# Kernel optimization log

Measured on AMD Instinct MI355X. Metric: run time of the kernel, lower is better.

## Reference

```python
import jax, jax.numpy as jnp
import numpy as np

BS, N = 8, 2000
ALPHA = 0.2  # LeakyReLU slope
NEG = -9e15


def _gat_head(x, adj, W, a):
    # x: [bs,N,Fin], W: [Fin,Fout], a: [2*Fout]
    h = x @ W                                   # [bs,N,F]
    F_ = W.shape[-1]
    # e_ij = lrelu(h_i . a[:F] + h_j . a[F:])  (decomposed form of concat+matmul)
    src = h @ a[:F_]                            # [bs,N]
    dst = h @ a[F_:]                            # [bs,N]
    e = jax.nn.leaky_relu(src[:, :, None] + dst[:, None, :], ALPHA)  # [bs,N,N]
    att = jnp.where(adj[None] > 0, e, NEG)
    att = jax.nn.softmax(att, axis=-1)
    return jax.nn.elu(att @ h)                  # [bs,N,F]


def _gat_multihead(x, adj, W, a):
    # W: [H,Fin,Fout], a: [H,2*Fout] -> concat heads on feature dim
    out = jax.vmap(_gat_head, in_axes=(None, None, 0, 0))(x, adj, W, a)  # [H,bs,N,F]
    H, bs, n, F_ = out.shape
    return jnp.moveaxis(out, 0, 2).reshape(bs, n, H * F_)


def setup_inputs() -> dict:
    key = jax.random.key(0)
    ks = jax.random.split(key, 20)
    g = 1.414

    def xavu(k, shape, gain=1.0):
        fan_in, fan_out = shape[-2], shape[-1]
        lim = gain * np.sqrt(6.0 / (fan_in + fan_out))
        return jax.random.uniform(k, shape, jnp.float32, -lim, lim)

    x = jax.random.normal(ks[0], (BS, N, 1), jnp.float32)
    adj = jax.random.randint(ks[1], (N, N), 0, 2).astype(jnp.float32)
    inp = {
        "x": x, "adj": adj,
        "W1": xavu(ks[2], (4, 1, 8), g), "a1": xavu(ks[3], (4, 16, 1), g)[..., 0],
        "W2": xavu(ks[4], (3, 32, 16), g), "a2": xavu(ks[5], (3, 32, 1), g)[..., 0],
        "pw1": xavu(ks[6], (32, 1))[:, 0], "pb1": jnp.zeros((1,), jnp.float32),
        "pw2": xavu(ks[7], (48, 1))[:, 0], "pb2": jnp.zeros((1,), jnp.float32),
        "fc1_w": xavu(ks[8], (3 * N, 600)), "fc1_b": jnp.zeros((600,), jnp.float32),
        "fc2_w": xavu(ks[9], (600, 256)), "fc2_b": jnp.zeros((256,), jnp.float32),
        "fc3_w": xavu(ks[10], (256, 64)), "fc3_b": jnp.zeros((64,), jnp.float32),
        "fc4_w": xavu(ks[11], (64, 32)), "fc4_b": jnp.zeros((32,), jnp.float32),
        "fc5_w": xavu(ks[12], (32, 2)), "fc5_b": jnp.zeros((2,), jnp.float32),
    }
    return inp


def reference(x, adj, W1, a1, W2, a2, pw1, pb1, pw2, pb2,
              fc1_w, fc1_b, fc2_w, fc2_b, fc3_w, fc3_b, fc4_w, fc4_b, fc5_w, fc5_b):
    # dropout layers are identity in eval mode
    x0 = jnp.mean(x, axis=-1)                       # [bs,N]
    h = _gat_multihead(x, adj, W1, a1)              # [bs,N,32]
    x1 = h @ pw1 + pb1                              # [bs,N]
    h = _gat_multihead(h, adj, W2, a2)              # [bs,N,48]
    x2 = h @ pw2 + pb2                              # [bs,N]
    z = jnp.concatenate([x0, x1, x2], axis=1)       # [bs,3N]
    z = jax.nn.elu(z @ fc1_w + fc1_b)
    z = jax.nn.elu(z @ fc2_w + fc2_b)
    z1 = jax.nn.elu(z @ fc3_w + fc3_b)              # output [bs,64]
    z = jax.nn.elu(z1 @ fc4_w + fc4_b)
    gat_out = z @ fc5_w + fc5_b                     # [bs,2]
    return (z1, gat_out)
```

## Files before the change

### kernel.cpp

```cpp
#include <hip/hip_runtime.h>
#include <hip/hip_bf16.h>
#include <cmath>

#define N_NODES 2000
#define BS 8

typedef __attribute__((ext_vector_type(8))) short short8v;
typedef __attribute__((ext_vector_type(4))) float float4v;

__device__ __forceinline__ float elu_f(float v) { return v > 0.f ? v : expm1f(v); }

__device__ __forceinline__ unsigned short f32_bf16u(float f) {
    __hip_bfloat16 h = __float2bfloat16(f);
    unsigned short u;
    __builtin_memcpy(&u, &h, 2);
    return u;
}
__device__ __forceinline__ short f32_bf16(float f) { return (short)f32_bf16u(f); }

__device__ __forceinline__ float sel_mask(float w, unsigned long long m) {
    float r;
    asm("v_cndmask_b32 %0, 0, %1, %2" : "=v"(r) : "v"(w), "s"(m));
    return r;
}

__global__ __launch_bounds__(256) void pack_kernel(
    const float* __restrict__ adj,
    unsigned long long* __restrict__ maskT, unsigned* __restrict__ maskT32,
    short* __restrict__ hT) {
    int bx = blockIdx.x;
    int tid = threadIdx.x;
    if (bx < N_NODES) {
        int row = bx;
        int lane = tid & 63, wv = tid >> 6;
        for (int wq = wv; wq < 32; wq += 4) {
            int j = wq * 64 + lane;
            bool on = (j < N_NODES) && (adj[(size_t)row * N_NODES + j] > 0.f);
            unsigned long long bal = __ballot(on);
            if (lane == 0) {
                maskT[(size_t)wq * 2048 + row] = bal;
                maskT32[(size_t)(2 * wq) * 2048 + row] = (unsigned)bal;
                maskT32[(size_t)(2 * wq + 1) * 2048 + row] = (unsigned)(bal >> 32);
            }
        }
        return;
    }
    for (int i = tid; i < 24 * 16 * 48; i += 256) {
        int bh = i / 768, rem = i % 768, f = rem / 48, n = N_NODES + rem % 48;
        hT[((size_t)bh * 16 + f) * 2048 + n] = 0;
    }
}

__global__ __launch_bounds__(256) void att1_kernel(
    const unsigned long long* __restrict__ maskT,
    const float* __restrict__ x,
    const float* __restrict__ W1, const float* __restrict__ a1,
    float* __restrict__ o1) {
    __shared__ unsigned sPQ[2][2048];
    __shared__ float sX[2048];
    __shared__ float2 redmm[256];
    int tid = threadIdx.x;
    int by = blockIdx.y, b = blockIdx.z;

    float mn = 1e30f, mx = -1e30f;
    for (int n = tid; n < 2048; n += 256) {
        float xv = (n < N_NODES) ? x[(size_t)b * N_NODES + n] : 0.f;
        sX[n] = xv;
        if (n < N_NODES) { mn = fminf(mn, xv); mx = fmaxf(mx, xv); }
    }
    redmm[tid] = make_float2(mn, mx);
    __syncthreads();
    for (int s = 128; s > 0; s >>= 1) {
        if (tid < s) {
            redmm[tid].x = fminf(redmm[tid].x, redmm[tid + s].x);
            redmm[tid].y = fmaxf(redmm[tid].y, redmm[tid + s].y);
        }
        __syncthreads();
    }
    float xmin = redmm[0].x, xmax = redmm[0].y;

    float wsv[2], wdv[2], md[2];
    #pragma unroll
    for (int hh = 0; hh < 2; ++hh) {
        int head = by * 2 + hh;
        float ws = 0.f, wd = 0.f;
        #pragma unroll
        for (int f = 0; f < 8; ++f) {
            float wv = W1[head * 8 + f];
            ws = fmaf(wv, a1[head * 16 + f], ws);
            wd = fmaf(wv, a1[head * 16 + 8 + f], wd);
        }
        wsv[hh] = ws; wdv[hh] = wd;
        md[hh] = wd >= 0.f ? wd * xmax : wd * xmin;
    }

    for (int n = tid; n < 2048; n += 256) {
        float xv = sX[n];
        #pragma unroll
        for (int hh = 0; hh < 2; ++hh) {
            unsigned v = 0;
            if (n < N_NODES) {
                float d = wdv[hh] * xv - md[hh];
                unsigned Pb = f32_bf16u(__expf(d));
                unsigned Qb = f32_bf16u(__expf(0.2f * d));
                v = (Pb << 16) | Qb;
            }
            sPQ[hh][n] = v;
        }
    }
    __syncthreads();

    int lane = tid & 63;
    int wave = __builtin_amdgcn_readfirstlane(tid >> 6);
    int t = blockIdx.x * 4 + wave;
    if (t >= 250) return;
    int row0 = t * 8;

    float A_[2][8], B_[2][8], num[2][8], den[2][8];
    #pragma unroll
    for (int hh = 0; hh < 2; ++hh) {
        #pragma unroll
        for (int r = 0; r < 8; ++r) {
            float sv = wsv[hh] * sX[row0 + r];
            float u = sv + md[hh], ub = fmaxf(u, 0.2f * u);
            A_[hh][r] = __expf(u - ub);
            B_[hh][r] = __expf(0.2f * u - ub);
            num[hh][r] = 0.f; den[hh][r] = 0.f;
        }
    }

    for (int j0 = 0; j0 < 2048; j0 += 64) {
        int j = j0 + lane;
        unsigned pq0 = sPQ[0][j];
        unsigned pq1 = sPQ[1][j];
        float xv = sX[j];
        float P0 = __uint_as_float(pq0 & 0xFFFF0000u);
        float Q0 = __uint_as_float(pq0 << 16);
        float P1 = __uint_as_float(pq1 & 0xFFFF0000u);
        float Q1 = __uint_as_float(pq1 << 16);
        const unsigned long long* mrow = maskT + ((size_t)(j0 >> 6) << 11) + row0;
        #pragma unroll
        for (int r = 0; r < 8; ++r) {
            unsigned long long m = mrow[r];
            float w0 = fmaxf(A_[0][r] * P0, B_[0][r] * Q0);
            w0 = sel_mask(w0, m);
            num[0][r] = fmaf(w0, xv, num[0][r]);
            den[0][r] += w0;
            float w1 = fmaxf(A_[1][r] * P1, B_[1][r] * Q1);
            w1 = sel_mask(w1, m);
            num[1][r] = fmaf(w1, xv, num[1][r]);
            den[1][r] += w1;
        }
    }
    #pragma unroll
    for (int off = 32; off >= 1; off >>= 1) {
        #pragma unroll
        for (int hh = 0; hh < 2; ++hh) {
            #pragma unroll
            for (int r = 0; r < 8; ++r) {
                num[hh][r] += __shfl_xor(num[hh][r], off, 64);
                den[hh][r] += __shfl_xor(den[hh][r], off, 64);
            }
        }
    }
    if (lane < 8) {
        #pragma unroll
        for (int hh = 0; hh < 2; ++hh) {
            int head = by * 2 + hh;
            float wf = W1[head * 8 + lane];
            #pragma unroll
            for (int r = 0; r < 8; ++r) {
                float ratio = den[hh][r] > 0.f ? num[hh][r] / den[hh][r] : 0.f;
                float v = ratio * wf;
                o1[((size_t)(b * N_NODES + row0 + r)) * 32 + head * 8 + lane] =
                    v > 0.f ? v : expm1f(v);
            }
        }
    }
}

__global__ __launch_bounds__(256) void prep2_kernel(
    const float* __restrict__ o1, const float* __restrict__ W2,
    const float* __restrict__ a2,
    short* __restrict__ hT, float* __restrict__ s2, float* __restrict__ d2) {
    __shared__ float sW[1536];
    int tid = threadIdx.x;
    for (int i = tid; i < 1536; i += 256) sW[i] = W2[i];
    __syncthreads();
    int idx = blockIdx.x * 256 + tid;
    if (idx >= BS * 3 * N_NODES) return;
    int b = idx / 6000, r = idx % 6000, h = r / N_NODES, n = r % N_NODES;
    int bh = b * 3 + h;
    float in[32];
    const float4* ip = (const float4*)(o1 + ((size_t)b * N_NODES + n) * 32);
    #pragma unroll
    for (int q = 0; q < 8; ++q) {
        float4 v = ip[q];
        in[4 * q] = v.x; in[4 * q + 1] = v.y; in[4 * q + 2] = v.z; in[4 * q + 3] = v.w;
    }
    float hv[16];
    #pragma unroll
    for (int f = 0; f < 16; ++f) hv[f] = 0.f;
    #pragma unroll
    for (int k = 0; k < 32; ++k) {
        float ik = in[k];
        #pragma unroll
        for (int f = 0; f < 16; ++f) hv[f] = fmaf(ik, sW[h * 512 + k * 16 + f], hv[f]);
    }
    float sr = 0.f, ds = 0.f;
    #pragma unroll
    for (int f = 0; f < 16; ++f) {
        hT[((size_t)bh * 16 + f) * 2048 + n] = f32_bf16(hv[f]);
        sr = fmaf(hv[f], a2[h * 32 + f], sr);
        ds = fmaf(hv[f], a2[h * 32 + 16 + f], ds);
    }
    s2[(size_t)bh * N_NODES + n] = sr;
    d2[(size_t)bh * N_NODES + n] = ds;
}

__global__ __launch_bounds__(256) void att2_kernel(
    const unsigned* __restrict__ maskT32,
    const short* __restrict__ hT,
    const float* __restrict__ s2, const float* __restrict__ d2,
    float* __restrict__ o2) {
    __shared__ float2 sPQ[2048];
    __shared__ float red[256];
    int tid = threadIdx.x;
    int head = blockIdx.y, b = blockIdx.z, bh = b * 3 + head;
    const float* dp = d2 + (size_t)bh * N_NODES;

    float mx = -1e30f;
    for (int n = tid; n < N_NODES; n += 256) mx = fmaxf(mx, dp[n]);
    red[tid] = mx;
    __syncthreads();
    for (int s = 128; s > 0; s >>= 1) {
        if (tid < s) red[tid] = fmaxf(red[tid], red[tid + s]);
        __syncthreads();
    }
    float md = red[0];
    for (int n = tid; n < 2048; n += 256) {
        if (n < N_NODES) {
            float d = dp[n] - md;
            sPQ[n] = make_float2(__expf(d), __expf(0.2f * d));
        } else {
            sPQ[n] = make_float2(0.f, 0.f);
        }
    }
    __syncthreads();

    int lane = tid & 63;
    int wave = __builtin_amdgcn_readfirstlane(tid >> 6);
    int t = blockIdx.x * 4 + wave;
    if (t >= 125) return;
    int rs = lane & 15;
    int g = lane >> 4;
    int row = t * 16 + rs;

    float sv = s2[(size_t)bh * N_NODES + row];
    float u = sv + md, ub = fmaxf(u, 0.2f * u);
    float Ar = __expf(u - ub), Br = __expf(0.2f * u - ub);
    const short* hb = hT + ((size_t)bh * 16 + rs) * 2048;

    float4v acc = {0.f, 0.f, 0.f, 0.f};
    float den = 0.f;

    for (int jc = 0; jc < 64; ++jc) {
        int jb = jc * 32 + g * 8;
        float w[8];
        #pragma unroll
        for (int e2 = 0; e2 < 4; ++e2) {
            float4 pq2 = *(const float4*)(&sPQ[jb + e2 * 2]);
            w[e2 * 2 + 0] = fmaxf(Ar * pq2.x, Br * pq2.y);
            w[e2 * 2 + 1] = fmaxf(Ar * pq2.z, Br * pq2.w);
        }
        unsigned mby = maskT32[(size_t)jc * 2048 + row] >> (g * 8);
        short8v av;
        #pragma unroll
        for (int e = 0; e < 8; ++e) {
            float we = (mby & (1u << e)) ? w[e] : 0.f;
            den += we;
            av[e] = f32_bf16(we);
        }
        short8v bv = *(const short8v*)(hb + jb);
        acc = __builtin_amdgcn_mfma_f32_16x16x32_bf16(av, bv, acc, 0, 0, 0);
    }

    den += __shfl_xor(den, 16, 64);
    den += __shfl_xor(den, 32, 64);
    float inv = den > 0.f ? 1.0f / den : 0.f;

    #pragma unroll
    for (int reg = 0; reg < 4; ++reg) {
        int crow = g * 4 + reg;
        float invr = __shfl(inv, crow, 64);
        float v = acc[reg] * invr;
        v = v > 0.f ? v : expm1f(v);
        o2[((size_t)(b * N_NODES + t * 16 + crow)) * 48 + head * 16 + rs] = v;
    }
}

__global__ __launch_bounds__(256) void fc1_splitk_kernel(
    const float* __restrict__ x,
    const float* __restrict__ o1, const float* __restrict__ o2,
    const float* __restrict__ pw1, const float* __restrict__ pb1,
    const float* __restrict__ pw2, const float* __restrict__ pb2,
    const float* __restrict__ W, float* __restrict__ partial) {
    const int K = 6000, O = 600, KS = 71;
    __shared__ float sz[BS][KS];
    int tid = threadIdx.x;
    int kt = blockIdx.y;
    int k0 = kt * KS;
    int len = (k0 + KS <= K) ? KS : (K - k0);
    float pb1v = pb1[0], pb2v = pb2[0];
    for (int i = tid; i < BS * len; i += 256) {
        int bb = i / len, k = k0 + i % len;
        float v;
        if (k < 2000) {
            v = x[bb * 2000 + k];
        } else if (k < 4000) {
            const float* op = o1 + ((size_t)bb * 2000 + (k - 2000)) * 32;
            float s = pb1v;
            #pragma unroll
            for (int q = 0; q < 32; ++q) s = fmaf(op[q], pw1[q], s);
            v = s;
        } else {
            const float* op = o2 + ((size_t)bb * 2000 + (k - 4000)) * 48;
            float s = pb2v;
            #pragma unroll
            for (int q = 0; q < 48; ++q) s = fmaf(op[q], pw2[q], s);
            v = s;
        }
        sz[bb][i % len] = v;
    }
    __syncthreads();
    int o = blockIdx.x * 256 + tid;
    float acc[BS] = {0.f, 0.f, 0.f, 0.f, 0.f, 0.f, 0.f, 0.f};
    if (o < O) {
        for (int k = 0; k < len; ++k) {
            float w = W[(size_t)(k0 + k) * O + o];
            #pragma unroll
            for (int b = 0; b < BS; ++b) acc[b] = fmaf(sz[b][k], w, acc[b]);
        }
        #pragma unroll
        for (int b = 0; b < BS; ++b)
            partial[((size_t)kt * BS + b) * O + o] = acc[b];
    }
}

__global__ __launch_bounds__(256) void fc2_splitk_kernel(
    const float* __restrict__ p1, const float* __restrict__ b1,
    const float* __restrict__ W, float* __restrict__ partial) {
    const int K = 600, O = 256, KS = 38;
    __shared__ float sz[BS][KS];
    int tid = threadIdx.x;
    int kt = blockIdx.y;
    int k0 = kt * KS;
    int k1 = k0 + KS < K ? k0 + KS : K;
    int len = k1 - k0;
    for (int i = tid; i < BS * len; i += 256) {
        int bb = i / len, k = k0 + i % len;
        float a = b1[k];
        #pragma unroll 5
        for (int q = 0; q < 85; ++q) a += p1[((size_t)q * BS + bb) * 600 + k];
        sz[bb][i % len] = elu_f(a);
    }
    __syncthreads();
    int o = tid;
    float acc[BS] = {0.f, 0.f, 0.f, 0.f, 0.f, 0.f, 0.f, 0.f};
    for (int k = 0; k < len; ++k) {
        float w = W[(size_t)(k0 + k) * O + o];
        #pragma unroll
        for (int b = 0; b < BS; ++b) acc[b] = fmaf(sz[b][k], w, acc[b]);
    }
    #pragma unroll
    for (int b = 0; b < BS; ++b)
        partial[((size_t)kt * BS + b) * O + o] = acc[b];
}

__global__ __launch_bounds__(256) void fc_tail_kernel(
    const float* __restrict__ p2, const float* __restrict__ b2,
    const float* __restrict__ w3, const float* __restrict__ b3,
    const float* __restrict__ w4, const float* __restrict__ b4,
    const float* __restrict__ w5, const float* __restrict__ b5,
    float* __restrict__ outp) {
    int b = blockIdx.x, tid = threadIdx.x;
    __shared__ float t2[256], red[256], z1[64], z4[32];
    {
        float a = b2[tid];
        #pragma unroll
        for (int kt = 0; kt < 16; ++kt) a += p2[((size_t)kt * BS + b) * 256 + tid];
        t2[tid] = elu_f(a);
    }
    __syncthreads();
    {
        int o = tid & 63, ks = tid >> 6;
        float a = 0.f;
        for (int k = ks; k < 256; k += 4) a = fmaf(t2[k], w3[k * 64 + o], a);
        red[tid] = a;
        __syncthreads();
        if (ks == 0) {
            float v = red[o] + red[64 + o] + red[128 + o] + red[192 + o] + b3[o];
            v = elu_f(v);
            z1[o] = v;
            outp[b * 64 + o] = v;
        }
    }
    __syncthreads();
    if (tid < 32) {
        float v = b4[tid];
        #pragma unroll
        for (int k = 0; k < 64; ++k) v = fmaf(z1[k], w4[k * 32 + tid], v);
        z4[tid] = elu_f(v);
    }
    __syncthreads();
    if (tid < 2) {
        float v = b5[tid];
        #pragma unroll
        for (int k = 0; k < 32; ++k) v = fmaf(z4[k], w5[k * 2 + tid], v);
        outp[BS * 64 + b * 2 + tid] = v;
    }
}

extern "C" void kernel_launch(void* const* d_in, const int* in_sizes, int n_in,
                              void* d_out, int out_size, void* d_ws, size_t ws_size,
                              hipStream_t stream) {
    const float* x    = (const float*)d_in[0];
    const float* adj  = (const float*)d_in[1];
    const float* W1   = (const float*)d_in[2];
    const float* a1   = (const float*)d_in[3];
    const float* W2   = (const float*)d_in[4];
    const float* a2   = (const float*)d_in[5];
    const float* pw1  = (const float*)d_in[6];
    const float* pb1  = (const float*)d_in[7];
    const float* pw2  = (const float*)d_in[8];
    const float* pb2  = (const float*)d_in[9];
    const float* fc1w = (const float*)d_in[10];
    const float* fc1b = (const float*)d_in[11];
    const float* fc2w = (const float*)d_in[12];
    const float* fc2b = (const float*)d_in[13];
    const float* fc3w = (const float*)d_in[14];
    const float* fc3b = (const float*)d_in[15];
    const float* fc4w = (const float*)d_in[16];
    const float* fc4b = (const float*)d_in[17];
    const float* fc5w = (const float*)d_in[18];
    const float* fc5b = (const float*)d_in[19];
    float* outp = (float*)d_out;

    float* ws = (float*)d_ws;
    size_t off = 0;
    auto alloc = [&](size_t n) {
        float* p = ws + off;
        off += (n + 63) & ~(size_t)63;
        return p;
    };
    float* o1 = alloc((size_t)BS * N_NODES * 32);
    float* s2 = alloc((size_t)24 * N_NODES);
    float* d2 = alloc((size_t)24 * N_NODES);
    short* hT = (short*)alloc((size_t)24 * 16 * 2048 / 2);
    float* o2 = alloc((size_t)BS * N_NODES * 48);
    const int KT1 = 85;
    float* p1 = alloc((size_t)KT1 * BS * 600);
    float* p2 = alloc((size_t)16 * BS * 256);
    unsigned long long* maskT = (unsigned long long*)alloc((size_t)32 * 2048 * 2);
    unsigned* maskT32 = (unsigned*)alloc((size_t)64 * 2048);

    pack_kernel<<<N_NODES + 1, 256, 0, stream>>>(adj, maskT, maskT32, hT);
    att1_kernel<<<dim3(63, 2, BS), 256, 0, stream>>>(maskT, x, W1, a1, o1);
    prep2_kernel<<<(BS * 3 * N_NODES + 255) / 256, 256, 0, stream>>>(o1, W2, a2, hT, s2, d2);
    att2_kernel<<<dim3(32, 3, BS), 256, 0, stream>>>(maskT32, hT, s2, d2, o2);
    fc1_splitk_kernel<<<dim3(3, KT1), 256, 0, stream>>>(
        x, o1, o2, pw1, pb1, pw2, pb2, fc1w, p1);
    fc2_splitk_kernel<<<dim3(1, 16), 256, 0, stream>>>(p1, fc1b, fc2w, p2);
    fc_tail_kernel<<<BS, 256, 0, stream>>>(
        p2, fc2b, fc3w, fc3b, fc4w, fc4b, fc5w, fc5b, outp);
}
```

Before: 136.1 us.

## Compute first-layer GAT attention aggregation with bf16 MFMA instead of scalar FMAs

The first attention layer now gives each block a single head. Each wave handles 16 rows and builds masked, unnormalised attention weights as a bf16 A operand, then uses a 16x16x32 bf16 MFMA against a B operand made of x values and a ones column, so numerator and denominator come out together. This replaces the per-lane scalar FMA loop and the long shuffle reduction, and the 64-bit mask array is dropped in favour of the existing 32-bit mask layout. In exchange the weights and x are rounded to bf16 before accumulation, and three quarters of the MFMA output columns are wasted.

```diff
diff --git a/kernel.cpp b/kernel.cpp
--- a/kernel.cpp
+++ b/kernel.cpp
@@ -18,15 +18,9 @@
 }
 __device__ __forceinline__ short f32_bf16(float f) { return (short)f32_bf16u(f); }
 
-__device__ __forceinline__ float sel_mask(float w, unsigned long long m) {
-    float r;
-    asm("v_cndmask_b32 %0, 0, %1, %2" : "=v"(r) : "v"(w), "s"(m));
-    return r;
-}
-
 __global__ __launch_bounds__(256) void pack_kernel(
     const float* __restrict__ adj,
-    unsigned long long* __restrict__ maskT, unsigned* __restrict__ maskT32,
+    unsigned* __restrict__ maskT32,
     short* __restrict__ hT) {
     int bx = blockIdx.x;
     int tid = threadIdx.x;
@@ -38,7 +32,6 @@
             bool on = (j < N_NODES) && (adj[(size_t)row * N_NODES + j] > 0.f);
             unsigned long long bal = __ballot(on);
             if (lane == 0) {
-                maskT[(size_t)wq * 2048 + row] = bal;
                 maskT32[(size_t)(2 * wq) * 2048 + row] = (unsigned)bal;
                 maskT32[(size_t)(2 * wq + 1) * 2048 + row] = (unsigned)(bal >> 32);
             }
@@ -52,20 +45,28 @@
 }
 
 __global__ __launch_bounds__(256) void att1_kernel(
-    const unsigned long long* __restrict__ maskT,
+    const unsigned* __restrict__ maskT32,
     const float* __restrict__ x,
     const float* __restrict__ W1, const float* __restrict__ a1,
     float* __restrict__ o1) {
-    __shared__ unsigned sPQ[2][2048];
-    __shared__ float sX[2048];
+    __shared__ float2 sPQ[2048];
+    __shared__ short sXb[2048];
     __shared__ float2 redmm[256];
     int tid = threadIdx.x;
-    int by = blockIdx.y, b = blockIdx.z;
+    int head = blockIdx.y, b = blockIdx.z;
+
+    float ws = 0.f, wd = 0.f;
+    #pragma unroll
+    for (int f = 0; f < 8; ++f) {
+        float wv = W1[head * 8 + f];
+        ws = fmaf(wv, a1[head * 16 + f], ws);
+        wd = fmaf(wv, a1[head * 16 + 8 + f], wd);
+    }
 
     float mn = 1e30f, mx = -1e30f;
     for (int n = tid; n < 2048; n += 256) {
         float xv = (n < N_NODES) ? x[(size_t)b * N_NODES + n] : 0.f;
-        sX[n] = xv;
+        sXb[n] = f32_bf16(xv);
         if (n < N_NODES) { mn = fminf(mn, xv); mx = fmaxf(mx, xv); }
     }
     redmm[tid] = make_float2(mn, mx);
@@ -77,35 +78,14 @@
         }
         __syncthreads();
     }
-    float xmin = redmm[0].x, xmax = redmm[0].y;
-
-    float wsv[2], wdv[2], md[2];
-    #pragma unroll
-    for (int hh = 0; hh < 2; ++hh) {
-        int head = by * 2 + hh;
-        float ws = 0.f, wd = 0.f;
-        #pragma unroll
-        for (int f = 0; f < 8; ++f) {
-            float wv = W1[head * 8 + f];
-            ws = fmaf(wv, a1[head * 16 + f], ws);
-            wd = fmaf(wv, a1[head * 16 + 8 + f], wd);
-        }
-        wsv[hh] = ws; wdv[hh] = wd;
-        md[hh] = wd >= 0.f ? wd * xmax : wd * xmin;
-    }
+    float md = wd >= 0.f ? wd * redmm[0].y : wd * redmm[0].x;
 
     for (int n = tid; n < 2048; n += 256) {
-        float xv = sX[n];
-        #pragma unroll
-        for (int hh = 0; hh < 2; ++hh) {
-            unsigned v = 0;
-            if (n < N_NODES) {
-                float d = wdv[hh] * xv - md[hh];
-                unsigned Pb = f32_bf16u(__expf(d));
-                unsigned Qb = f32_bf16u(__expf(0.2f * d));
-                v = (Pb << 16) | Qb;
-            }
-            sPQ[hh][n] = v;
+        if (n < N_NODES) {
+            float d = wd * x[(size_t)b * N_NODES + n] - md;
+            sPQ[n] = make_float2(__expf(d), __expf(0.2f * d));
+        } else {
+            sPQ[n] = make_float2(0.f, 0.f);
         }
     }
     __syncthreads();
@@ -113,68 +93,57 @@
     int lane = tid & 63;
     int wave = __builtin_amdgcn_readfirstlane(tid >> 6);
     int t = blockIdx.x * 4 + wave;
-    if (t >= 250) return;
-    int row0 = t * 8;
-
-    float A_[2][8], B_[2][8], num[2][8], den[2][8];
-    #pragma unroll
-    for (int hh = 0; hh < 2; ++hh) {
-        #pragma unroll
-        for (int r = 0; r < 8; ++r) {
-            float sv = wsv[hh] * sX[row0 + r];
-            float u = sv + md[hh], ub = fmaxf(u, 0.2f * u);
-            A_[hh][r] = __expf(u - ub);
-            B_[hh][r] = __expf(0.2f * u - ub);
-            num[hh][r] = 0.f; den[hh][r] = 0.f;
-        }
-    }
-
-    for (int j0 = 0; j0 < 2048; j0 += 64) {
-        int j = j0 + lane;
-        unsigned pq0 = sPQ[0][j];
-        unsigned pq1 = sPQ[1][j];
-        float xv = sX[j];
-        float P0 = __uint_as_float(pq0 & 0xFFFF0000u);
-        float Q0 = __uint_as_float(pq0 << 16);
-        float P1 = __uint_as_float(pq1 & 0xFFFF0000u);
-        float Q1 = __uint_as_float(pq1 << 16);
-        const unsigned long long* mrow = maskT + ((size_t)(j0 >> 6) << 11) + row0;
-        #pragma unroll
-        for (int r = 0; r < 8; ++r) {
-            unsigned long long m = mrow[r];
-            float w0 = fmaxf(A_[0][r] * P0, B_[0][r] * Q0);
-            w0 = sel_mask(w0, m);
-            num[0][r] = fmaf(w0, xv, num[0][r]);
-            den[0][r] += w0;
-            float w1 = fmaxf(A_[1][r] * P1, B_[1][r] * Q1);
-            w1 = sel_mask(w1, m);
-            num[1][r] = fmaf(w1, xv, num[1][r]);
-            den[1][r] += w1;
-        }
-    }
-    #pragma unroll
-    for (int off = 32; off >= 1; off >>= 1) {
-        #pragma unroll
-        for (int hh = 0; hh < 2; ++hh) {
-            #pragma unroll
-            for (int r = 0; r < 8; ++r) {
-                num[hh][r] += __shfl_xor(num[hh][r], off, 64);
-                den[hh][r] += __shfl_xor(den[hh][r], off, 64);
-            }
-        }
-    }
-    if (lane < 8) {
-        #pragma unroll
-        for (int hh = 0; hh < 2; ++hh) {
-            int head = by * 2 + hh;
-            float wf = W1[head * 8 + lane];
-            #pragma unroll
-            for (int r = 0; r < 8; ++r) {
-                float ratio = den[hh][r] > 0.f ? num[hh][r] / den[hh][r] : 0.f;
-                float v = ratio * wf;
-                o1[((size_t)(b * N_NODES + row0 + r)) * 32 + head * 8 + lane] =
-                    v > 0.f ? v : expm1f(v);
-            }
+    if (t >= 125) return;
+    int rs = lane & 15;
+    int g = lane >> 4;
+    int row = t * 16 + rs;
+
+    float xr = x[(size_t)b * N_NODES + row];
+    float u = ws * xr + md, ub = fmaxf(u, 0.2f * u);
+    float Ar = __expf(u - ub), Br = __expf(0.2f * u - ub);
+
+    unsigned fill = (rs == 1) ? 0x3F803F80u : 0u;
+    bool isx = (rs == 0);
+
+    float4v acc = {0.f, 0.f, 0.f, 0.f};
+
+    for (int jc = 0; jc < 64; ++jc) {
+        int jb = jc * 32 + g * 8;
+        float w[8];
+        #pragma unroll
+        for (int e2 = 0; e2 < 4; ++e2) {
+            float4 pq2 = *(const float4*)(&sPQ[jb + e2 * 2]);
+            w[e2 * 2 + 0] = fmaxf(Ar * pq2.x, Br * pq2.y);
+            w[e2 * 2 + 1] = fmaxf(Ar * pq2.z, Br * pq2.w);
+        }
+        unsigned mby = maskT32[(size_t)jc * 2048 + row] >> (g * 8);
+        short8v av;
+        #pragma unroll
+        for (int e = 0; e < 8; ++e) {
+            float we = (mby & (1u << e)) ? w[e] : 0.f;
+            av[e] = f32_bf16(we);
+        }
+        uint4 xv4 = *(const uint4*)(sXb + jb);
+        uint4 bu;
+        bu.x = isx ? xv4.x : fill;
+        bu.y = isx ? xv4.y : fill;
+        bu.z = isx ? xv4.z : fill;
+        bu.w = isx ? xv4.w : fill;
+        short8v bv;
+        __builtin_memcpy(&bv, &bu, 16);
+        acc = __builtin_amdgcn_mfma_f32_16x16x32_bf16(av, bv, acc, 0, 0, 0);
+    }
+
+    #pragma unroll
+    for (int reg = 0; reg < 4; ++reg) {
+        int crow = g * 4 + reg;
+        float nm = __shfl(acc[reg], lane & 48, 64);
+        float dn = __shfl(acc[reg], (lane & 48) | 1, 64);
+        float ratio = dn > 0.f ? nm / dn : 0.f;
+        if (rs < 8) {
+            float v = ratio * W1[head * 8 + rs];
+            v = v > 0.f ? v : expm1f(v);
+            o1[((size_t)(b * N_NODES + t * 16 + crow)) * 32 + head * 8 + rs] = v;
         }
     }
 }
@@ -461,11 +430,10 @@
     const int KT1 = 85;
     float* p1 = alloc((size_t)KT1 * BS * 600);
     float* p2 = alloc((size_t)16 * BS * 256);
-    unsigned long long* maskT = (unsigned long long*)alloc((size_t)32 * 2048 * 2);
     unsigned* maskT32 = (unsigned*)alloc((size_t)64 * 2048);
 
-    pack_kernel<<<N_NODES + 1, 256, 0, stream>>>(adj, maskT, maskT32, hT);
-    att1_kernel<<<dim3(63, 2, BS), 256, 0, stream>>>(maskT, x, W1, a1, o1);
+    pack_kernel<<<N_NODES + 1, 256, 0, stream>>>(adj, maskT32, hT);
+    att1_kernel<<<dim3(32, 4, BS), 256, 0, stream>>>(maskT32, x, W1, a1, o1);
     prep2_kernel<<<(BS * 3 * N_NODES + 255) / 256, 256, 0, stream>>>(o1, W2, a2, hT, s2, d2);
     att2_kernel<<<dim3(32, 3, BS), 256, 0, stream>>>(maskT32, hT, s2, d2, o2);
     fc1_splitk_kernel<<<dim3(3, KT1), 256, 0, stream>>>(
```

Measured after the change: 131.2 us. 1.04x faster.
